# Kernel optimization log

Hardware: AMD Instinct MI355X
Metric: run time of the kernel (lower is better)

Reference implementation:

```python
import jax, jax.numpy as jnp
import numpy as np

B, N, DIM, HEADS, DIM_HEAD = 2, 2048, 1024, 16, 64
INNER = HEADS * DIM_HEAD
LN_EPS = 1e-5


def setup_inputs() -> dict:
    key = jax.random.key(0)
    k1, k2, k3 = jax.random.split(key, 3)
    x = jax.random.normal(k1, (B, N, DIM), dtype=jnp.float32)
    ln_w = jnp.ones((DIM,), dtype=jnp.float32)
    ln_b = jnp.zeros((DIM,), dtype=jnp.float32)
    w_qkv = jax.random.normal(k2, (DIM, 3 * INNER), dtype=jnp.float32) * (DIM ** -0.5)
    w_out = jax.random.normal(k3, (INNER, DIM), dtype=jnp.float32) * (INNER ** -0.5)
    return {"x": x, "ln_w": ln_w, "ln_b": ln_b, "w_qkv": w_qkv, "w_out": w_out}


def reference(x, ln_w, ln_b, w_qkv, w_out):
    scale = DIM_HEAD ** -0.5
    # LayerNorm over last dim
    mu = jnp.mean(x, axis=-1, keepdims=True)
    var = jnp.var(x, axis=-1, keepdims=True)
    xn = (x - mu) / jnp.sqrt(var + LN_EPS) * ln_w + ln_b
    # qkv projection, split, reshape to b h n d
    qkv = xn @ w_qkv  # [B, N, 3*INNER]
    q, k, v = jnp.split(qkv, 3, axis=-1)
    def to_heads(t):
        return t.reshape(B, N, HEADS, DIM_HEAD).transpose(0, 2, 1, 3)
    q, k, v = to_heads(q) * scale, to_heads(k), to_heads(v)
    # scores + causal mask (triu with offset 1 masked)
    sim = jnp.einsum('bhid,bhjd->bhij', q, k)  # [B, H, N, N]
    causal_mask = jnp.triu(jnp.ones((N, N), dtype=bool), k=1)
    sim = jnp.where(causal_mask, -jnp.finfo(sim.dtype).max, sim)
    attn = jax.nn.softmax(sim, axis=-1)
    out = jnp.einsum('bhij,bhjd->bhid', attn, v)  # [B, H, N, D]
    out = out.transpose(0, 2, 1, 3).reshape(B, N, INNER)
    return out @ w_out
```

## Files before the change

kernel.cpp:

```cpp
#include <hip/hip_runtime.h>
#include <stdint.h>

#define BATCH 2
#define NSEQ  2048
#define DIMC  1024
#define NHEAD 16
#define DHEAD 64
#define QKVN  3072
#define MROWS 4096

typedef __attribute__((ext_vector_type(8))) unsigned short u16x8;
typedef __attribute__((ext_vector_type(4))) unsigned short u16x4;
typedef __attribute__((ext_vector_type(8))) short          bf16x8;
typedef __attribute__((ext_vector_type(4))) float          f32x4;

#define F32_PROBE 0x3F800000u
#define QSCALE 0.18033688f

__device__ __forceinline__ float b2f(unsigned short u) {
  union { unsigned int i; float f; } c; c.i = ((unsigned int)u) << 16; return c.f;
}
__device__ __forceinline__ unsigned short f2b(float f) {
  unsigned int u = __float_as_uint(f);
  return (unsigned short)((u + 0x7fffu + ((u >> 16) & 1u)) >> 16);
}
__device__ __forceinline__ float fast_exp2(float x) {
  return __builtin_amdgcn_exp2f(x);
}
__device__ __forceinline__ void async16(const unsigned short* g, unsigned short* s) {
  __builtin_amdgcn_global_load_lds(
      (const __attribute__((address_space(1))) unsigned int*)g,
      (__attribute__((address_space(3))) unsigned int*)s, 16, 0, 0);
}

__device__ __forceinline__ void tr_tile(const void* __restrict__ in,
                                        unsigned short* __restrict__ out,
                                        int R, int C, int r0, int c0, bool f32,
                                        int t, unsigned short (*tile)[33],
                                        int scale_below) {
  int tx = t & 31, ty = t >> 5;
  float sc = (c0 < scale_below) ? QSCALE : 1.0f;
  if (f32) {
    #pragma unroll
    for (int i = 0; i < 32; i += 8)
      tile[ty + i][tx] = f2b(((const float*)in)[(size_t)(r0 + ty + i) * C + c0 + tx] * sc);
  } else {
    #pragma unroll
    for (int i = 0; i < 32; i += 8)
      tile[ty + i][tx] = f2b(b2f(((const unsigned short*)in)[(size_t)(r0 + ty + i) * C + c0 + tx]) * sc);
  }
  __syncthreads();
  #pragma unroll
  for (int i = 0; i < 32; i += 8)
    out[(size_t)(c0 + ty + i) * R + r0 + tx] = tile[tx][ty + i];
}

__global__ __launch_bounds__(256) void prep_kernel(const void* __restrict__ x,
                                                   const void* __restrict__ w,
                                                   const void* __restrict__ bb,
                                                   unsigned short* __restrict__ xn,
                                                   const void* __restrict__ w_qkv,
                                                   unsigned short* __restrict__ wqkvT,
                                                   const void* __restrict__ w_out,
                                                   unsigned short* __restrict__ woutT,
                                                   const unsigned int* __restrict__ probe) {
  __shared__ unsigned short tile[32][33];
  __shared__ float red[8];
  bool f32 = (*probe == F32_PROBE);
  int bid = blockIdx.x, t = threadIdx.x;

  if (bid < MROWS) {
    int row = bid;
    float v0, v1, v2, v3, w0, w1, w2, w3, bb0, bb1, bb2, bb3;
    if (f32) {
      const float* xr = (const float*)x + (size_t)row * DIMC;
      float4 xv = *(const float4*)(xr + t * 4);
      v0 = xv.x; v1 = xv.y; v2 = xv.z; v3 = xv.w;
      float4 wv = *(const float4*)((const float*)w + t * 4);
      w0 = wv.x; w1 = wv.y; w2 = wv.z; w3 = wv.w;
      float4 bv = *(const float4*)((const float*)bb + t * 4);
      bb0 = bv.x; bb1 = bv.y; bb2 = bv.z; bb3 = bv.w;
    } else {
      const unsigned short* xr = (const unsigned short*)x + (size_t)row * DIMC;
      u16x4 xv = *(const u16x4*)(xr + t * 4);
      v0 = b2f(xv[0]); v1 = b2f(xv[1]); v2 = b2f(xv[2]); v3 = b2f(xv[3]);
      u16x4 wv = *(const u16x4*)((const unsigned short*)w + t * 4);
      w0 = b2f(wv[0]); w1 = b2f(wv[1]); w2 = b2f(wv[2]); w3 = b2f(wv[3]);
      u16x4 bv = *(const u16x4*)((const unsigned short*)bb + t * 4);
      bb0 = b2f(bv[0]); bb1 = b2f(bv[1]); bb2 = b2f(bv[2]); bb3 = b2f(bv[3]);
    }
    float s = v0 + v1 + v2 + v3;
    float q = v0 * v0 + v1 * v1 + v2 * v2 + v3 * v3;
    #pragma unroll
    for (int off = 1; off < 64; off <<= 1) { s += __shfl_xor(s, off); q += __shfl_xor(q, off); }
    int wv_ = t >> 6;
    if ((t & 63) == 0) { red[wv_] = s; red[4 + wv_] = q; }
    __syncthreads();
    s = red[0] + red[1] + red[2] + red[3];
    q = red[4] + red[5] + red[6] + red[7];
    float mu  = s * (1.0f / DIMC);
    float var = q * (1.0f / DIMC) - mu * mu;
    float rstd = rsqrtf(var + 1e-5f);
    u16x4 o;
    o[0] = f2b((v0 - mu) * rstd * w0 + bb0);
    o[1] = f2b((v1 - mu) * rstd * w1 + bb1);
    o[2] = f2b((v2 - mu) * rstd * w2 + bb2);
    o[3] = f2b((v3 - mu) * rstd * w3 + bb3);
    *(u16x4*)(xn + (size_t)row * DIMC + t * 4) = o;
  } else if (bid < MROWS + 3072) {
    int tid = bid - MROWS;
    tr_tile(w_qkv, wqkvT, DIMC, QKVN, (tid / 96) * 32, (tid % 96) * 32, f32, t, tile, 1024);
  } else {
    int tid = bid - (MROWS + 3072);
    tr_tile(w_out, woutT, DIMC, DIMC, (tid >> 5) * 32, (tid & 31) * 32, f32, t, tile, 0);
  }
}

__global__ __launch_bounds__(256) void transpose_kernel(const void* __restrict__ in,
                                                        unsigned short* __restrict__ out,
                                                        int R, int C,
                                                        const unsigned int* __restrict__ probe) {
  __shared__ unsigned short tile[32][33];
  bool f32 = (*probe == F32_PROBE);
  int t = threadIdx.x;
  tr_tile(in, out, R, C, blockIdx.y * 32, blockIdx.x * 32, f32, t, tile, 0);
}

__device__ __forceinline__ void ldA8(bf16x8 (&dst)[8], const unsigned short* base,
                                     int off, int ch0, int ch1) {
  #pragma unroll
  for (int mi = 0; mi < 4; ++mi) {
    dst[mi * 2 + 0] = *(const bf16x8*)&base[off + mi * 1024 + ch0];
    dst[mi * 2 + 1] = *(const bf16x8*)&base[off + mi * 1024 + ch1];
  }
}
__device__ __forceinline__ void ldB4(bf16x8 (&dst)[4], const unsigned short* base,
                                     int off, int ch0, int ch1) {
  #pragma unroll
  for (int ni = 0; ni < 2; ++ni) {
    dst[ni * 2 + 0] = *(const bf16x8*)&base[off + ni * 1024 + ch0];
    dst[ni * 2 + 1] = *(const bf16x8*)&base[off + ni * 1024 + ch1];
  }
}
__device__ __forceinline__ void mfma16q(f32x4 (&acc)[8][4], const bf16x8 (&a)[8],
                                        const bf16x8 (&b)[4], int R, int C) {
  #pragma unroll
  for (int kh = 0; kh < 2; ++kh)
    #pragma unroll
    for (int mi = 0; mi < 4; ++mi)
      #pragma unroll
      for (int ni = 0; ni < 2; ++ni)
        acc[R * 4 + mi][C * 2 + ni] = __builtin_amdgcn_mfma_f32_16x16x32_bf16(
            a[mi * 2 + kh], b[ni * 2 + kh], acc[R * 4 + mi][C * 2 + ni], 0, 0, 0);
}

#define SB    asm volatile("s_barrier" ::: "memory")
#define WVM4  asm volatile("s_waitcnt vmcnt(4)" ::: "memory")
#define WLG0  asm volatile("s_waitcnt lgkmcnt(0)" ::: "memory")
#define PRIO1 __builtin_amdgcn_s_setprio(1)
#define PRIO0 __builtin_amdgcn_s_setprio(0)
#define STG(gp, g, k0, sb) async16((gp) + (size_t)(g) * 65536 + (k0), (sb) + (g) * 4096 + t8)

__global__ __launch_bounds__(512) void gemm1_8p(const unsigned short* __restrict__ A,
                                                const unsigned short* __restrict__ Bt,
                                                unsigned short* __restrict__ C,
                                                unsigned short* __restrict__ vt_out) {
  __shared__ unsigned short lds[65536];
  unsigned short* A0b = lds;
  unsigned short* B0b = lds + 16384;
  unsigned short* A1b = lds + 32768;
  unsigned short* B1b = lds + 49152;

  int t = threadIdx.x;
  int lane = t & 63, wv = t >> 6;
  int l16 = lane & 15, quad = lane >> 4;
  int wr = wv >> 2, wc = wv & 3;

  int bid = blockIdx.x;
  int swzid = (bid & 7) * 24 + (bid >> 3);
  int bx = swzid / 12, by = swzid % 12;
  int bm = bx * 256, bn = by * 256;

  int rl = t >> 3;
  int sc8 = (((t & 7) ^ (rl & 7)) << 3);
  int t8 = t * 8;
  const unsigned short* Ag = A  + (size_t)(bm + rl) * 1024 + sc8;
  const unsigned short* Bg = Bt + (size_t)(bn + rl) * 1024 + sc8;

  int aoff = (wr * 128 + l16) * 64;
  int boff = (wc * 64 + l16) * 64;
  int ch0 = ((quad ^ (l16 & 7)) << 3);
  int ch1 = (((quad + 4) ^ (l16 & 7)) << 3);

  f32x4 acc[8][4] = {};
  bf16x8 ar0[8], ar1[8], bc0[4], bc1[4];

  STG(Ag, 0, 0, A0b); STG(Ag, 1, 0, A0b); STG(Ag, 2, 0, A0b); STG(Ag, 3, 0, A0b);
  STG(Bg, 0, 0, B0b); STG(Bg, 1, 0, B0b); STG(Bg, 2, 0, B0b); STG(Bg, 3, 0, B0b);
  STG(Ag, 0, 64, A1b); STG(Ag, 1, 64, A1b); STG(Ag, 2, 64, A1b); STG(Ag, 3, 64, A1b);
  WVM4;
  SB;

  for (int i = 0; i < 8; ++i) {
    const int k_b1 = (2 * i + 1) * 64;
    const int k_n0 = ((2 * i + 2) & 15) * 64;
    const int k_n1 = ((2 * i + 3) & 15) * 64;

    ldA8(ar0, A0b, aoff, ch0, ch1);
    ldB4(bc0, B0b, boff, ch0, ch1);
    STG(Bg, 0, k_b1, B1b); STG(Bg, 1, k_b1, B1b);
    SB; WLG0; PRIO1; mfma16q(acc, ar0, bc0, 0, 0); PRIO0; SB;
    ldA8(ar1, A0b, aoff + 4096, ch0, ch1);
    STG(Bg, 2, k_b1, B1b); STG(Bg, 3, k_b1, B1b);
    SB; WLG0; PRIO1; mfma16q(acc, ar1, bc0, 1, 0); PRIO0; SB;
    ldB4(bc1, B0b, boff + 2048, ch0, ch1);
    STG(Ag, 0, k_n0, A0b); STG(Ag, 1, k_n0, A0b);
    SB; WLG0; PRIO1; mfma16q(acc, ar0, bc1, 0, 1); PRIO0; SB;
    STG(Ag, 2, k_n0, A0b); STG(Ag, 3, k_n0, A0b);
    WVM4;
    SB; PRIO1; mfma16q(acc, ar1, bc1, 1, 1); PRIO0; SB;

    ldA8(ar0, A1b, aoff, ch0, ch1);
    ldB4(bc0, B1b, boff, ch0, ch1);
    STG(Bg, 0, k_n0, B0b); STG(Bg, 1, k_n0, B0b);
    SB; WLG0; PRIO1; mfma16q(acc, ar0, bc0, 0, 0); PRIO0; SB;
    ldA8(ar1, A1b, aoff + 4096, ch0, ch1);
    STG(Bg, 2, k_n0, B0b); STG(Bg, 3, k_n0, B0b);
    SB; WLG0; PRIO1; mfma16q(acc, ar1, bc0, 1, 0); PRIO0; SB;
    ldB4(bc1, B1b, boff + 2048, ch0, ch1);
    STG(Ag, 0, k_n1, A1b); STG(Ag, 1, k_n1, A1b);
    SB; WLG0; PRIO1; mfma16q(acc, ar0, bc1, 0, 1); PRIO0; SB;
    STG(Ag, 2, k_n1, A1b); STG(Ag, 3, k_n1, A1b);
    WVM4;
    SB; PRIO1; mfma16q(acc, ar1, bc1, 1, 1); PRIO0; SB;
  }

  bool vblk = (bn >= 2048);
  #pragma unroll
  for (int rf = 0; rf < 8; ++rf)
    #pragma unroll
    for (int cf = 0; cf < 4; ++cf) {
      int gr0 = bm + wr * 128 + rf * 16 + quad * 4;
      int gc  = bn + wc * 64 + cf * 16 + l16;
      if (vblk) {
        int hh = (gc >> 6) & 15;
        int dd = gc & 63;
        int bb2 = gr0 >> 11;
        int n0  = gr0 & 2047;
        u16x4 pk;
        #pragma unroll
        for (int r = 0; r < 4; r++) pk[r] = f2b(acc[rf][cf][r]);
        *(u16x4*)&vt_out[(((size_t)(bb2 * 16 + hh) * 64 + dd) << 11) + n0] = pk;
      } else {
        #pragma unroll
        for (int r = 0; r < 4; r++)
          C[(size_t)(gr0 + r) * QKVN + gc] = f2b(acc[rf][cf][r]);
      }
    }
}

__global__ __launch_bounds__(256) void gemm_bt_n64(const unsigned short* __restrict__ A,
                                                   const unsigned short* __restrict__ Bt,
                                                   void* __restrict__ Cv,
                                                   int M, int N, int K, int lda,
                                                   int detect_out,
                                                   const unsigned int* __restrict__ probe) {
  __shared__ unsigned short As[128 * 32];
  __shared__ unsigned short Bs[64 * 32];
  int t = threadIdx.x;
  int lane = t & 63, wave = t >> 6;
  int l16 = lane & 15, quad = lane >> 4;
  int wm = (wave & 1) * 64, wn = (wave >> 1) * 32;
  int bm = blockIdx.x * 128, bn = blockIdx.y * 64;

  f32x4 acc[4][2] = {};

  int srow = t >> 2;
  int scol = (t & 3) * 8;
  const unsigned short* Ap = A  + (size_t)(bm + srow) * lda + scol;
  const unsigned short* Bp = Bt + (size_t)(bn + srow) * K + scol;
  unsigned short* As0 = &As[srow * 32 + scol];
  unsigned short* As1 = &As[(64 + srow) * 32 + scol];
  unsigned short* Bs0 = &Bs[srow * 32 + scol];

  for (int k0 = 0; k0 < K; k0 += 32) {
    __syncthreads();
    async16(Ap + k0, As0);
    async16(Ap + (size_t)64 * lda + k0, As1);
    async16(Bp + k0, Bs0);
    __syncthreads();
    bf16x8 af[4], bfr[2];
    #pragma unroll
    for (int mi = 0; mi < 4; mi++)
      af[mi] = *(const bf16x8*)&As[(wm + mi * 16 + l16) * 32 + quad * 8];
    #pragma unroll
    for (int ni = 0; ni < 2; ni++)
      bfr[ni] = *(const bf16x8*)&Bs[(wn + ni * 16 + l16) * 32 + quad * 8];
    #pragma unroll
    for (int mi = 0; mi < 4; mi++)
      #pragma unroll
      for (int ni = 0; ni < 2; ni++)
        acc[mi][ni] = __builtin_amdgcn_mfma_f32_16x16x32_bf16(af[mi], bfr[ni], acc[mi][ni], 0, 0, 0);
  }
  bool f32out = detect_out && (*probe == F32_PROBE);
  #pragma unroll
  for (int mi = 0; mi < 4; mi++)
    #pragma unroll
    for (int ni = 0; ni < 2; ni++)
      #pragma unroll
      for (int r = 0; r < 4; r++) {
        int gr = bm + wm + mi * 16 + quad * 4 + r;
        int gc = bn + wn + ni * 16 + l16;
        if (f32out) ((float*)Cv)[(size_t)gr * N + gc] = acc[mi][ni][r];
        else ((unsigned short*)Cv)[(size_t)gr * N + gc] = f2b(acc[mi][ni][r]);
      }
}

__device__ __forceinline__ int swz(int row, int chunk) {
  return row * 64 + ((chunk ^ (row & 7)) << 3);
}

__global__ __launch_bounds__(256) void attn_v4(unsigned short* __restrict__ qkv,
                                               const unsigned short* __restrict__ vt) {
  __shared__ unsigned short lds[20480];

  int t = threadIdx.x;
  int lane = t & 63, w = t >> 6;
  int l16 = lane & 15, quad = lane >> 4;
  int pair = blockIdx.x;
  int bh = blockIdx.y;
  int b = bh >> 4, h = bh & 15;
  unsigned short* qbase = qkv + (size_t)(b * NSEQ) * QKVN + h * DHEAD;
  const unsigned short* kbase = qbase + 1024;
  const unsigned short* vtb = vt + (size_t)bh * DHEAD * NSEQ;
  unsigned short* Ps = lds + 16384;

  int sr = t >> 3, sc = t & 7;

  for (int ph = 0; ph < 2; ph++) {
    int qt = ph ? pair : 31 - pair;
    int q0 = qt * 64;

    const unsigned short* qp = qbase + (size_t)(q0 + w * 16 + l16) * QKVN + quad * 8;
    bf16x8 bq0 = *(const bf16x8*)(qp);
    bf16x8 bq1 = *(const bf16x8*)(qp + 32);

    float l_i = 0.f;
    f32x4 o[4] = {};
    u16x8 k0r, k1r, v0r, v1r;

    if (ph) __syncthreads();

    k0r = *(const u16x8*)(kbase + (size_t)sr * QKVN + sc * 8);
    k1r = *(const u16x8*)(kbase + (size_t)(sr + 32) * QKVN + sc * 8);
    v0r = *(const u16x8*)(vtb + (size_t)sr * NSEQ + sc * 8);
    v1r = *(const u16x8*)(vtb + (size_t)(sr + 32) * NSEQ + sc * 8);
    *(u16x8*)&lds[swz(sr, sc)]             = k0r;
    *(u16x8*)&lds[swz(sr + 32, sc)]        = k1r;
    *(u16x8*)&lds[8192 + swz(sr, sc)]      = v0r;
    *(u16x8*)&lds[8192 + swz(sr + 32, sc)] = v1r;
    __syncthreads();

    for (int jt = 0; jt <= qt; jt++) {
      const unsigned short* Kc = lds + (jt & 1) * 4096;
      const unsigned short* Vc = lds + 8192 + (jt & 1) * 4096;

      if (jt < qt) {
        int j0n = (jt + 1) * 64;
        k0r = *(const u16x8*)(kbase + (size_t)(j0n + sr) * QKVN + sc * 8);
        k1r = *(const u16x8*)(kbase + (size_t)(j0n + sr + 32) * QKVN + sc * 8);
        v0r = *(const u16x8*)(vtb + (size_t)sr * NSEQ + j0n + sc * 8);
        v1r = *(const u16x8*)(vtb + (size_t)(sr + 32) * NSEQ + j0n + sc * 8);
      }

      f32x4 s[4];
      #pragma unroll
      for (int mj = 0; mj < 4; mj++)
        #pragma unroll
        for (int r = 0; r < 4; r++) s[mj][r] = -32.0f;
      #pragma unroll
      for (int mj = 0; mj < 4; mj++) {
        bf16x8 ak0 = *(const bf16x8*)&Kc[swz(mj * 16 + l16, quad)];
        s[mj] = __builtin_amdgcn_mfma_f32_16x16x32_bf16(ak0, bq0, s[mj], 0, 0, 0);
        bf16x8 ak1 = *(const bf16x8*)&Kc[swz(mj * 16 + l16, 4 + quad)];
        s[mj] = __builtin_amdgcn_mfma_f32_16x16x32_bf16(ak1, bq1, s[mj], 0, 0, 0);
      }

      if (jt == qt) {
        int il = w * 16 + l16;
        #pragma unroll
        for (int mj = 0; mj < 4; mj++)
          #pragma unroll
          for (int r = 0; r < 4; r++)
            if (mj * 16 + quad * 4 + r > il) s[mj][r] = -1e30f;
      }

      #pragma unroll
      for (int mj = 0; mj < 4; mj++) {
        u16x4 pk;
        #pragma unroll
        for (int r = 0; r < 4; r++) {
          float p = fast_exp2(s[mj][r]);
          l_i += p;
          pk[r] = f2b(p);
        }
        int ch = mj * 2 + (quad >> 1);
        *(u16x4*)&Ps[swz(w * 16 + l16, ch) + (quad & 1) * 4] = pk;
      }

      #pragma unroll
      for (int ks = 0; ks < 2; ks++) {
        bf16x8 ap = *(const bf16x8*)&Ps[swz(w * 16 + l16, ks * 4 + quad)];
        #pragma unroll
        for (int d = 0; d < 4; d++) {
          bf16x8 bv = *(const bf16x8*)&Vc[swz(d * 16 + l16, ks * 4 + quad)];
          o[d] = __builtin_amdgcn_mfma_f32_16x16x32_bf16(ap, bv, o[d], 0, 0, 0);
        }
      }

      if (jt < qt) {
        unsigned short* Kn = lds + ((jt + 1) & 1) * 4096;
        unsigned short* Vn = lds + 8192 + ((jt + 1) & 1) * 4096;
        *(u16x8*)&Kn[swz(sr, sc)]      = k0r;
        *(u16x8*)&Kn[swz(sr + 32, sc)] = k1r;
        *(u16x8*)&Vn[swz(sr, sc)]      = v0r;
        *(u16x8*)&Vn[swz(sr + 32, sc)] = v1r;
        __syncthreads();
      }
    }

    l_i += __shfl_xor(l_i, 16);
    l_i += __shfl_xor(l_i, 32);
    #pragma unroll
    for (int r = 0; r < 4; r++) {
      float lr = __shfl(l_i, (lane & 48) | (quad * 4 + r));
      float inv = 1.0f / lr;
      int row = q0 + w * 16 + quad * 4 + r;
      #pragma unroll
      for (int d = 0; d < 4; d++)
        qbase[(size_t)row * QKVN + d * 16 + l16] = f2b(o[d][r] * inv);
    }
  }
}

extern "C" void kernel_launch(void* const* d_in, const int* in_sizes, int n_in,
                              void* d_out, int out_size, void* d_ws, size_t ws_size,
                              hipStream_t stream) {
  const void* x     = d_in[0];
  const void* ln_w  = d_in[1];
  const void* ln_b  = d_in[2];
  const void* w_qkv = d_in[3];
  const void* w_out = d_in[4];
  const unsigned int* probe = (const unsigned int*)d_in[1];

  unsigned short* wqkvT = (unsigned short*)d_ws;
  unsigned short* qkv   = wqkvT + (size_t)QKVN * DIMC;
  unsigned short* xn    = (unsigned short*)d_out;
  size_t base_e  = (size_t)QKVN * DIMC + (size_t)MROWS * QKVN;
  size_t vt_e    = (size_t)BATCH * NHEAD * DHEAD * NSEQ;
  size_t wout_e  = (size_t)DIMC * DIMC;
  bool fit_vt  = ws_size >= (base_e + vt_e) * 2;
  bool fit_all = ws_size >= (base_e + vt_e + wout_e) * 2;
  unsigned short* vtp   = fit_vt ? qkv + (size_t)MROWS * QKVN
                                 : ((unsigned short*)d_out) + ((size_t)4 * 1024 * 1024);
  unsigned short* woutT = fit_all ? vtp + vt_e : wqkvT;

  int prep_blocks = MROWS + 3072 + (fit_all ? 1024 : 0);
  prep_kernel<<<prep_blocks, 256, 0, stream>>>(x, ln_w, ln_b, xn, w_qkv, wqkvT,
                                               w_out, fit_all ? woutT : nullptr, probe);
  gemm1_8p<<<dim3(192), 512, 0, stream>>>(xn, wqkvT, qkv, vtp);
  if (!fit_all)
    transpose_kernel<<<dim3(DIMC / 32, DIMC / 32), 256, 0, stream>>>(w_out, woutT, DIMC, DIMC, probe);
  attn_v4<<<dim3(NSEQ / 128, BATCH * NHEAD), 256, 0, stream>>>(qkv, vtp);
  gemm_bt_n64<<<dim3(MROWS / 128, DIMC / 64), 256, 0, stream>>>(
      qkv, woutT, d_out, MROWS, DIMC, DIMC, QKVN, 1, probe);
}
```

Baseline: 182.1 us.

## Double-buffer output GEMM and split attention into one tile per block

The output-projection GEMM now double-buffers its LDS tiles, so each k-step's async load overlaps the MFMAs on the previous tile and only one barrier is needed per iteration. The attention kernel no longer processes a pair of query tiles per block. It launches 1024 single-tile blocks, ordered longest-first and mapped so consecutive block IDs land on different XCDs by batch-head. Scheduling-priority hints are placed around the MFMA sections. The aim is better load balance and memory/compute overlap, at the cost of more blocks that each reload K/V and higher LDS use in the GEMM.

Result: no change. 180.3 us (-1.0%).

```diff
diff --git a/kernel.cpp b/kernel.cpp
--- a/kernel.cpp
+++ b/kernel.cpp
@@ -265,8 +265,8 @@
                                                    int M, int N, int K, int lda,
                                                    int detect_out,
                                                    const unsigned int* __restrict__ probe) {
-  __shared__ unsigned short As[128 * 32];
-  __shared__ unsigned short Bs[64 * 32];
+  __shared__ unsigned short As[2][128 * 32];
+  __shared__ unsigned short Bs[2][64 * 32];
   int t = threadIdx.x;
   int lane = t & 63, wave = t >> 6;
   int l16 = lane & 15, quad = lane >> 4;
@@ -279,28 +279,37 @@
   int scol = (t & 3) * 8;
   const unsigned short* Ap = A  + (size_t)(bm + srow) * lda + scol;
   const unsigned short* Bp = Bt + (size_t)(bn + srow) * K + scol;
-  unsigned short* As0 = &As[srow * 32 + scol];
-  unsigned short* As1 = &As[(64 + srow) * 32 + scol];
-  unsigned short* Bs0 = &Bs[srow * 32 + scol];
-
+  int so0 = srow * 32 + scol;
+  int so1 = (64 + srow) * 32 + scol;
+
+  async16(Ap, &As[0][so0]);
+  async16(Ap + (size_t)64 * lda, &As[0][so1]);
+  async16(Bp, &Bs[0][so0]);
+  __syncthreads();
+
+  int cur = 0;
   for (int k0 = 0; k0 < K; k0 += 32) {
-    __syncthreads();
-    async16(Ap + k0, As0);
-    async16(Ap + (size_t)64 * lda + k0, As1);
-    async16(Bp + k0, Bs0);
-    __syncthreads();
+    if (k0 + 32 < K) {
+      async16(Ap + k0 + 32, &As[cur ^ 1][so0]);
+      async16(Ap + (size_t)64 * lda + k0 + 32, &As[cur ^ 1][so1]);
+      async16(Bp + k0 + 32, &Bs[cur ^ 1][so0]);
+    }
     bf16x8 af[4], bfr[2];
     #pragma unroll
     for (int mi = 0; mi < 4; mi++)
-      af[mi] = *(const bf16x8*)&As[(wm + mi * 16 + l16) * 32 + quad * 8];
+      af[mi] = *(const bf16x8*)&As[cur][(wm + mi * 16 + l16) * 32 + quad * 8];
     #pragma unroll
     for (int ni = 0; ni < 2; ni++)
-      bfr[ni] = *(const bf16x8*)&Bs[(wn + ni * 16 + l16) * 32 + quad * 8];
+      bfr[ni] = *(const bf16x8*)&Bs[cur][(wn + ni * 16 + l16) * 32 + quad * 8];
+    PRIO1;
     #pragma unroll
     for (int mi = 0; mi < 4; mi++)
       #pragma unroll
       for (int ni = 0; ni < 2; ni++)
         acc[mi][ni] = __builtin_amdgcn_mfma_f32_16x16x32_bf16(af[mi], bfr[ni], acc[mi][ni], 0, 0, 0);
+    PRIO0;
+    __syncthreads();
+    cur ^= 1;
   }
   bool f32out = detect_out && (*probe == F32_PROBE);
   #pragma unroll
@@ -320,15 +329,17 @@
   return row * 64 + ((chunk ^ (row & 7)) << 3);
 }
 
-__global__ __launch_bounds__(256) void attn_v4(unsigned short* __restrict__ qkv,
+__global__ __launch_bounds__(256) void attn_v5(unsigned short* __restrict__ qkv,
                                                const unsigned short* __restrict__ vt) {
   __shared__ unsigned short lds[20480];
 
   int t = threadIdx.x;
   int lane = t & 63, w = t >> 6;
   int l16 = lane & 15, quad = lane >> 4;
-  int pair = blockIdx.x;
-  int bh = blockIdx.y;
+  int id = blockIdx.x;
+  int xcd = id & 7, jj = id >> 3;
+  int bh = xcd + ((jj & 3) << 3);
+  int qt = 31 - (jj >> 2);
   int b = bh >> 4, h = bh & 15;
   unsigned short* qbase = qkv + (size_t)(b * NSEQ) * QKVN + h * DHEAD;
   const unsigned short* kbase = qbase + 1024;
@@ -336,110 +347,108 @@
   unsigned short* Ps = lds + 16384;
 
   int sr = t >> 3, sc = t & 7;
-
-  for (int ph = 0; ph < 2; ph++) {
-    int qt = ph ? pair : 31 - pair;
-    int q0 = qt * 64;
-
-    const unsigned short* qp = qbase + (size_t)(q0 + w * 16 + l16) * QKVN + quad * 8;
-    bf16x8 bq0 = *(const bf16x8*)(qp);
-    bf16x8 bq1 = *(const bf16x8*)(qp + 32);
-
-    float l_i = 0.f;
-    f32x4 o[4] = {};
-    u16x8 k0r, k1r, v0r, v1r;
-
-    if (ph) __syncthreads();
-
-    k0r = *(const u16x8*)(kbase + (size_t)sr * QKVN + sc * 8);
-    k1r = *(const u16x8*)(kbase + (size_t)(sr + 32) * QKVN + sc * 8);
-    v0r = *(const u16x8*)(vtb + (size_t)sr * NSEQ + sc * 8);
-    v1r = *(const u16x8*)(vtb + (size_t)(sr + 32) * NSEQ + sc * 8);
-    *(u16x8*)&lds[swz(sr, sc)]             = k0r;
-    *(u16x8*)&lds[swz(sr + 32, sc)]        = k1r;
-    *(u16x8*)&lds[8192 + swz(sr, sc)]      = v0r;
-    *(u16x8*)&lds[8192 + swz(sr + 32, sc)] = v1r;
-    __syncthreads();
-
-    for (int jt = 0; jt <= qt; jt++) {
-      const unsigned short* Kc = lds + (jt & 1) * 4096;
-      const unsigned short* Vc = lds + 8192 + (jt & 1) * 4096;
-
-      if (jt < qt) {
-        int j0n = (jt + 1) * 64;
-        k0r = *(const u16x8*)(kbase + (size_t)(j0n + sr) * QKVN + sc * 8);
-        k1r = *(const u16x8*)(kbase + (size_t)(j0n + sr + 32) * QKVN + sc * 8);
-        v0r = *(const u16x8*)(vtb + (size_t)sr * NSEQ + j0n + sc * 8);
-        v1r = *(const u16x8*)(vtb + (size_t)(sr + 32) * NSEQ + j0n + sc * 8);
-      }
-
-      f32x4 s[4];
+  int q0 = qt * 64;
+
+  const unsigned short* qp = qbase + (size_t)(q0 + w * 16 + l16) * QKVN + quad * 8;
+  bf16x8 bq0 = *(const bf16x8*)(qp);
+  bf16x8 bq1 = *(const bf16x8*)(qp + 32);
+
+  float l_i = 0.f;
+  f32x4 o[4] = {};
+  u16x8 k0r, k1r, v0r, v1r;
+
+  k0r = *(const u16x8*)(kbase + (size_t)sr * QKVN + sc * 8);
+  k1r = *(const u16x8*)(kbase + (size_t)(sr + 32) * QKVN + sc * 8);
+  v0r = *(const u16x8*)(vtb + (size_t)sr * NSEQ + sc * 8);
+  v1r = *(const u16x8*)(vtb + (size_t)(sr + 32) * NSEQ + sc * 8);
+  *(u16x8*)&lds[swz(sr, sc)]             = k0r;
+  *(u16x8*)&lds[swz(sr + 32, sc)]        = k1r;
+  *(u16x8*)&lds[8192 + swz(sr, sc)]      = v0r;
+  *(u16x8*)&lds[8192 + swz(sr + 32, sc)] = v1r;
+  __syncthreads();
+
+  for (int jt = 0; jt <= qt; jt++) {
+    const unsigned short* Kc = lds + (jt & 1) * 4096;
+    const unsigned short* Vc = lds + 8192 + (jt & 1) * 4096;
+
+    if (jt < qt) {
+      int j0n = (jt + 1) * 64;
+      k0r = *(const u16x8*)(kbase + (size_t)(j0n + sr) * QKVN + sc * 8);
+      k1r = *(const u16x8*)(kbase + (size_t)(j0n + sr + 32) * QKVN + sc * 8);
+      v0r = *(const u16x8*)(vtb + (size_t)sr * NSEQ + j0n + sc * 8);
+      v1r = *(const u16x8*)(vtb + (size_t)(sr + 32) * NSEQ + j0n + sc * 8);
+    }
+
+    f32x4 s[4];
+    #pragma unroll
+    for (int mj = 0; mj < 4; mj++)
+      #pragma unroll
+      for (int r = 0; r < 4; r++) s[mj][r] = -32.0f;
+    PRIO1;
+    #pragma unroll
+    for (int mj = 0; mj < 4; mj++) {
+      bf16x8 ak0 = *(const bf16x8*)&Kc[swz(mj * 16 + l16, quad)];
+      s[mj] = __builtin_amdgcn_mfma_f32_16x16x32_bf16(ak0, bq0, s[mj], 0, 0, 0);
+      bf16x8 ak1 = *(const bf16x8*)&Kc[swz(mj * 16 + l16, 4 + quad)];
+      s[mj] = __builtin_amdgcn_mfma_f32_16x16x32_bf16(ak1, bq1, s[mj], 0, 0, 0);
+    }
+    PRIO0;
+
+    if (jt == qt) {
+      int il = w * 16 + l16;
       #pragma unroll
       for (int mj = 0; mj < 4; mj++)
         #pragma unroll
-        for (int r = 0; r < 4; r++) s[mj][r] = -32.0f;
-      #pragma unroll
-      for (int mj = 0; mj < 4; mj++) {
-        bf16x8 ak0 = *(const bf16x8*)&Kc[swz(mj * 16 + l16, quad)];
-        s[mj] = __builtin_amdgcn_mfma_f32_16x16x32_bf16(ak0, bq0, s[mj], 0, 0, 0);
-        bf16x8 ak1 = *(const bf16x8*)&Kc[swz(mj * 16 + l16, 4 + quad)];
-        s[mj] = __builtin_amdgcn_mfma_f32_16x16x32_bf16(ak1, bq1, s[mj], 0, 0, 0);
+        for (int r = 0; r < 4; r++)
+          if (mj * 16 + quad * 4 + r > il) s[mj][r] = -1e30f;
+    }
+
+    #pragma unroll
+    for (int mj = 0; mj < 4; mj++) {
+      u16x4 pk;
+      #pragma unroll
+      for (int r = 0; r < 4; r++) {
+        float p = fast_exp2(s[mj][r]);
+        l_i += p;
+        pk[r] = f2b(p);
       }
-
-      if (jt == qt) {
-        int il = w * 16 + l16;
-        #pragma unroll
-        for (int mj = 0; mj < 4; mj++)
-          #pragma unroll
-          for (int r = 0; r < 4; r++)
-            if (mj * 16 + quad * 4 + r > il) s[mj][r] = -1e30f;
+      int ch = mj * 2 + (quad >> 1);
+      *(u16x4*)&Ps[swz(w * 16 + l16, ch) + (quad & 1) * 4] = pk;
+    }
+
+    PRIO1;
+    #pragma unroll
+    for (int ks = 0; ks < 2; ks++) {
+      bf16x8 ap = *(const bf16x8*)&Ps[swz(w * 16 + l16, ks * 4 + quad)];
+      #pragma unroll
+      for (int d = 0; d < 4; d++) {
+        bf16x8 bv = *(const bf16x8*)&Vc[swz(d * 16 + l16, ks * 4 + quad)];
+        o[d] = __builtin_amdgcn_mfma_f32_16x16x32_bf16(ap, bv, o[d], 0, 0, 0);
       }
-
-      #pragma unroll
-      for (int mj = 0; mj < 4; mj++) {
-        u16x4 pk;
-        #pragma unroll
-        for (int r = 0; r < 4; r++) {
-          float p = fast_exp2(s[mj][r]);
-          l_i += p;
-          pk[r] = f2b(p);
-        }
-        int ch = mj * 2 + (quad >> 1);
-        *(u16x4*)&Ps[swz(w * 16 + l16, ch) + (quad & 1) * 4] = pk;
-      }
-
-      #pragma unroll
-      for (int ks = 0; ks < 2; ks++) {
-        bf16x8 ap = *(const bf16x8*)&Ps[swz(w * 16 + l16, ks * 4 + quad)];
-        #pragma unroll
-        for (int d = 0; d < 4; d++) {
-          bf16x8 bv = *(const bf16x8*)&Vc[swz(d * 16 + l16, ks * 4 + quad)];
-          o[d] = __builtin_amdgcn_mfma_f32_16x16x32_bf16(ap, bv, o[d], 0, 0, 0);
-        }
-      }
-
-      if (jt < qt) {
-        unsigned short* Kn = lds + ((jt + 1) & 1) * 4096;
-        unsigned short* Vn = lds + 8192 + ((jt + 1) & 1) * 4096;
-        *(u16x8*)&Kn[swz(sr, sc)]      = k0r;
-        *(u16x8*)&Kn[swz(sr + 32, sc)] = k1r;
-        *(u16x8*)&Vn[swz(sr, sc)]      = v0r;
-        *(u16x8*)&Vn[swz(sr + 32, sc)] = v1r;
-        __syncthreads();
-      }
-    }
-
-    l_i += __shfl_xor(l_i, 16);
-    l_i += __shfl_xor(l_i, 32);
-    #pragma unroll
-    for (int r = 0; r < 4; r++) {
-      float lr = __shfl(l_i, (lane & 48) | (quad * 4 + r));
-      float inv = 1.0f / lr;
-      int row = q0 + w * 16 + quad * 4 + r;
-      #pragma unroll
-      for (int d = 0; d < 4; d++)
-        qbase[(size_t)row * QKVN + d * 16 + l16] = f2b(o[d][r] * inv);
-    }
+    }
+    PRIO0;
+
+    if (jt < qt) {
+      unsigned short* Kn = lds + ((jt + 1) & 1) * 4096;
+      unsigned short* Vn = lds + 8192 + ((jt + 1) & 1) * 4096;
+      *(u16x8*)&Kn[swz(sr, sc)]      = k0r;
+      *(u16x8*)&Kn[swz(sr + 32, sc)] = k1r;
+      *(u16x8*)&Vn[swz(sr, sc)]      = v0r;
+      *(u16x8*)&Vn[swz(sr + 32, sc)] = v1r;
+      __syncthreads();
+    }
+  }
+
+  l_i += __shfl_xor(l_i, 16);
+  l_i += __shfl_xor(l_i, 32);
+  #pragma unroll
+  for (int r = 0; r < 4; r++) {
+    float lr = __shfl(l_i, (lane & 48) | (quad * 4 + r));
+    float inv = 1.0f / lr;
+    int row = q0 + w * 16 + quad * 4 + r;
+    #pragma unroll
+    for (int d = 0; d < 4; d++)
+      qbase[(size_t)row * QKVN + d * 16 + l16] = f2b(o[d][r] * inv);
   }
 }
 
@@ -471,7 +480,7 @@
   gemm1_8p<<<dim3(192), 512, 0, stream>>>(xn, wqkvT, qkv, vtp);
   if (!fit_all)
     transpose_kernel<<<dim3(DIMC / 32, DIMC / 32), 256, 0, stream>>>(w_out, woutT, DIMC, DIMC, probe);
-  attn_v4<<<dim3(NSEQ / 128, BATCH * NHEAD), 256, 0, stream>>>(qkv, vtp);
+  attn_v5<<<dim3(1024), 256, 0, stream>>>(qkv, vtp);
   gemm_bt_n64<<<dim3(MROWS / 128, DIMC / 64), 256, 0, stream>>>(
       qkv, woutT, d_out, MROWS, DIMC, DIMC, QKVN, 1, probe);
 }
```
